# Optimization experiments

Measured on AMD Instinct MI355X. Metric: run time of the kernel, lower is better.

The kernel has to match this reference:

```python
import jax, jax.numpy as jnp
import numpy as np

B, S, ENC, HID = 2, 2048, 2048, 2048
HQ, HKV, D = 8, 4, 256
SOFTCAP = 50.0
SCALING = float(256) ** -0.5  # query_pre_attn_scalar ** -0.5
EPS = 1e-6
NEG = -1e9  # finite stand-in for -inf in additive masks


def _rms_norm(x, w, eps=EPS):
    # GemmaRMSNorm: fp32 compute, scale by (1 + weight)
    xf = x.astype(jnp.float32)
    n = xf * jax.lax.rsqrt(jnp.mean(xf * xf, axis=-1, keepdims=True) + eps)
    return (n * (1.0 + w.astype(jnp.float32))).astype(x.dtype)


def _rotate_half(x):
    x1, x2 = jnp.split(x, 2, axis=-1)
    return jnp.concatenate([-x2, x1], axis=-1)


def _apply_rope(q, k, cos, sin):
    # q,k: [B, H, S, D]; cos,sin: [1, S, D] -> unsqueeze head dim
    c, s = cos[:, None, :, :], sin[:, None, :, :]
    return q * c + _rotate_half(q) * s, k * c + _rotate_half(k) * s


def setup_inputs() -> dict:
    key = jax.random.key(0)
    ks = jax.random.split(key, 8)
    hidden_states = jax.random.normal(ks[0], (B, S, HID), jnp.float32)
    encoder_hidden_states = jax.random.normal(ks[1], (B, ENC, HID), jnp.float32)
    # RoPE tables (base 10000)
    pos = jnp.arange(S, dtype=jnp.float32)
    inv_freq = 1.0 / (10000.0 ** (jnp.arange(0, D, 2, dtype=jnp.float32) / D))
    freqs = pos[:, None] * inv_freq[None, :]                 # [S, D/2]
    emb = jnp.concatenate([freqs, freqs], axis=-1)           # [S, D]
    cos = jnp.cos(emb)[None]                                 # [1, S, D]
    sin = jnp.sin(emb)[None]
    # merged additive mask: causal over self part, fully visible cross part
    causal = jnp.where(jnp.arange(S)[:, None] >= jnp.arange(S)[None, :], 0.0, NEG)
    mask = jnp.concatenate([causal, jnp.zeros((S, ENC), jnp.float32)], axis=-1)
    merged_attention_mask = mask[None, None].astype(jnp.float32)  # [1,1,S,S+ENC]
    w = 0.02
    Wq = jax.random.normal(ks[2], (HQ * D, HID), jnp.float32) * w
    Wk = jax.random.normal(ks[3], (HKV * D, HID), jnp.float32) * w
    Wv = jax.random.normal(ks[4], (HKV * D, HID), jnp.float32) * w
    Wo = jax.random.normal(ks[5], (HID, HQ * D), jnp.float32) * w
    q_norm_w = jnp.zeros((D,), jnp.float32)
    k_norm_w = jnp.zeros((D,), jnp.float32)
    return dict(hidden_states=hidden_states, encoder_hidden_states=encoder_hidden_states,
                cos=cos, sin=sin, merged_attention_mask=merged_attention_mask,
                Wq=Wq, Wk=Wk, Wv=Wv, Wo=Wo, q_norm_w=q_norm_w, k_norm_w=k_norm_w)


def reference(hidden_states, encoder_hidden_states, cos, sin, merged_attention_mask,
              Wq, Wk, Wv, Wo, q_norm_w, k_norm_w):
    b, s, _ = hidden_states.shape
    enc = encoder_hidden_states.shape[1]
    n_rep = HQ // HKV
    # projections
    q = hidden_states @ Wq.T                                 # [B,S,HQ*D]
    k_self = hidden_states @ Wk.T
    v_self = hidden_states @ Wv.T
    k_cross = encoder_hidden_states @ Wk.T
    v_cross = encoder_hidden_states @ Wv.T
    q = q.reshape(b, s, HQ, D).transpose(0, 2, 1, 3)         # [B,HQ,S,D]
    k_self = k_self.reshape(b, s, HKV, D).transpose(0, 2, 1, 3)
    v_self = v_self.reshape(b, s, HKV, D).transpose(0, 2, 1, 3)
    k_cross = k_cross.reshape(b, enc, HKV, D).transpose(0, 2, 1, 3)
    v_cross = v_cross.reshape(b, enc, HKV, D).transpose(0, 2, 1, 3)
    # QK RMSNorm + RoPE (RoPE only on self q/k)
    q = _rms_norm(q, q_norm_w)
    k_self = _rms_norm(k_self, k_norm_w)
    k_cross = _rms_norm(k_cross, k_norm_w)
    q, k_self = _apply_rope(q, k_self, cos, sin)
    # merged KV + GQA repeat
    k = jnp.concatenate([k_self, k_cross], axis=2)           # [B,HKV,S+ENC,D]
    v = jnp.concatenate([v_self, v_cross], axis=2)
    k = jnp.repeat(k, n_rep, axis=1)                         # [B,HQ,S+ENC,D]
    v = jnp.repeat(v, n_rep, axis=1)
    # eager softcapped attention
    scores = jnp.einsum('bhqd,bhkd->bhqk', q, k) * SCALING
    scores = SOFTCAP * jnp.tanh(scores / SOFTCAP)
    scores = scores + merged_attention_mask
    probs = jax.nn.softmax(scores, axis=-1)
    attn = jnp.einsum('bhqk,bhkd->bhqd', probs, v)           # [B,HQ,S,D]
    attn = attn.transpose(0, 2, 1, 3).reshape(b, s, HQ * D)
    return attn @ Wo.T
```

## Files before the change

kernel.cpp:

```cpp
#include <hip/hip_runtime.h>
#include <cstdint>

typedef __attribute__((ext_vector_type(8))) short bf16x8;
typedef __attribute__((ext_vector_type(4))) float f32x4;

#define B_ 2
#define S_ 2048
#define ENC_ 2048
#define HID_ 2048
#define HQ_ 8
#define HKV_ 4
#define D_ 256
#define L_ 4096

__device__ __forceinline__ short f2bf(float f) {
  uint32_t u = __builtin_bit_cast(uint32_t, f);
  u = (u + 0x7fffu + ((u >> 16) & 1u)) >> 16;
  return (short)u;
}
__device__ __forceinline__ float bf2f(short s) {
  uint32_t u = ((uint32_t)(uint16_t)s) << 16;
  return __builtin_bit_cast(float, u);
}

__device__ __forceinline__ void llds16(const void* g, void* s) {
  __builtin_amdgcn_global_load_lds(
      (const __attribute__((address_space(1))) void*)(__builtin_bit_cast(uintptr_t, g)),
      (__attribute__((address_space(3))) void*)(uint32_t)(__builtin_bit_cast(uintptr_t, s)),
      16, 0, 0);
}

__global__ __launch_bounds__(256) void cvt_f32_bf16(const float* __restrict__ in,
                                                    short* __restrict__ out, int n) {
  int i = (blockIdx.x * 256 + threadIdx.x) * 4;
  if (i >= n) return;
  float4 v = *(const float4*)(in + i);
  short4 r;
  r.x = f2bf(v.x); r.y = f2bf(v.y); r.z = f2bf(v.z); r.w = f2bf(v.w);
  *(short4*)(out + i) = r;
}

template <int BF16OUT>
__global__ __launch_bounds__(256, 2)
void gemm_bt(const short* __restrict__ A, const short* __restrict__ Bw,
             void* __restrict__ Cout, int M, int N, int K) {
  __shared__ __align__(16) short As[128 * 32];
  __shared__ __align__(16) short Bs[128 * 32];
  const int t = threadIdx.x;
  const int w = t >> 6;
  const int l = t & 63;
  const int lr = l & 15;
  const int lq = l >> 4;
  const int bm = blockIdx.y * 128;
  const int bn = blockIdx.x * 128;
  const int wm = (w & 1) * 64;
  const int wn = (w >> 1) * 64;

  f32x4 acc[4][4];
#pragma unroll
  for (int i = 0; i < 4; i++)
#pragma unroll
    for (int j = 0; j < 4; j++) acc[i][j] = f32x4{0.f, 0.f, 0.f, 0.f};

  const int srow = 32 * w + (l >> 2);
  const int scol = (l & 3) * 8;
  const short* gA = A + (size_t)(bm + srow) * K + scol;
  const short* gB = Bw + (size_t)(bn + srow) * K + scol;
  short* sA = &As[srow * 32 + scol];
  short* sB = &Bs[srow * 32 + scol];

  for (int k0 = 0; k0 < K; k0 += 32) {
    llds16(gA + k0, sA);
    llds16(gA + k0 + (size_t)16 * K, sA + 16 * 32);
    llds16(gB + k0, sB);
    llds16(gB + k0 + (size_t)16 * K, sB + 16 * 32);
    __syncthreads();
    bf16x8 af[4], bfr[4];
#pragma unroll
    for (int mi = 0; mi < 4; mi++)
      af[mi] = *(const bf16x8*)&As[(wm + 16 * mi + lr) * 32 + lq * 8];
#pragma unroll
    for (int ni = 0; ni < 4; ni++)
      bfr[ni] = *(const bf16x8*)&Bs[(wn + 16 * ni + lr) * 32 + lq * 8];
    __syncthreads();
#pragma unroll
    for (int mi = 0; mi < 4; mi++)
#pragma unroll
      for (int ni = 0; ni < 4; ni++)
        acc[mi][ni] =
            __builtin_amdgcn_mfma_f32_16x16x32_bf16(af[mi], bfr[ni], acc[mi][ni], 0, 0, 0);
  }

#pragma unroll
  for (int mi = 0; mi < 4; mi++)
#pragma unroll
    for (int ni = 0; ni < 4; ni++)
#pragma unroll
      for (int r = 0; r < 4; r++) {
        int row = bm + wm + 16 * mi + lq * 4 + r;
        int col = bn + wn + 16 * ni + lr;
        float v = acc[mi][ni][r];
        if (BF16OUT)
          ((short*)Cout)[(size_t)row * N + col] = f2bf(v);
        else
          ((float*)Cout)[(size_t)row * N + col] = v;
      }
}

__global__ __launch_bounds__(256)
void norm_rope(const short* __restrict__ src, int src_ld, int col0, int H,
               short* __restrict__ dst, int dstL, int pos_off, int do_rope, int kswz,
               const float* __restrict__ wn, const float* __restrict__ cosp,
               const float* __restrict__ sinp) {
  __shared__ float sh[256];
  __shared__ float red[4];
  int bid = blockIdx.x;
  int s = bid & (S_ - 1);
  int h = (bid >> 11) % H;
  int b = (bid >> 11) / H;
  int d = threadIdx.x;
  int w = d >> 6, l = d & 63;
  float x = bf2f(src[(size_t)(b * S_ + s) * src_ld + col0 + h * D_ + d]);
  float ss = x * x;
#pragma unroll
  for (int off = 32; off; off >>= 1) ss += __shfl_xor(ss, off, 64);
  if (l == 0) red[w] = ss;
  __syncthreads();
  float tot = red[0] + red[1] + red[2] + red[3];
  float y = x * rsqrtf(tot * (1.0f / D_) + 1e-6f) * (1.0f + wn[d]);
  float outv = y;
  if (do_rope) {
    sh[d] = y;
    __syncthreads();
    float c = cosp[s * D_ + d];
    float sn = sinp[s * D_ + d];
    outv = (d < 128) ? (y * c - sh[d + 128] * sn) : (y * c + sh[d - 128] * sn);
  }
  int dd = d;
  if (kswz) dd = (((d >> 3) ^ (s & 7)) << 3) | (d & 7);
  dst[((size_t)(b * H + h) * dstL + pos_off + s) * D_ + dd] = f2bf(outv);
}

__global__ __launch_bounds__(256)
void v_transpose(const short* __restrict__ qkv_self, const short* __restrict__ kv_cross,
                 short* __restrict__ Vt) {
  __shared__ __align__(16) short tile[64][72];
  int bid = blockIdx.x;
  int dt = bid & 3;
  int lt = (bid >> 2) & 63;
  int h = (bid >> 8) & 3;
  int b = bid >> 10;
  int t = threadIdx.x;
  int rl = t >> 2;
  int cc = (t & 3) * 16;
  int l = lt * 64 + rl;
  const short* src;
  if (lt < 32)
    src = qkv_self + (size_t)(b * S_ + l) * 4096 + 3072 + h * D_ + dt * 64 + cc;
  else
    src = kv_cross + (size_t)(b * ENC_ + (l - S_)) * 2048 + 1024 + h * D_ + dt * 64 + cc;
  *(bf16x8*)&tile[rl][cc] = *(const bf16x8*)src;
  *(bf16x8*)&tile[rl][cc + 8] = *(const bf16x8*)(src + 8);
  __syncthreads();
  int dl = t >> 2;
  int lc = (t & 3) * 16;
  bf16x8 v0, v1;
#pragma unroll
  for (int j = 0; j < 8; j++) {
    v0[j] = tile[lc + j][dl];
    v1[j] = tile[lc + 8 + j][dl];
  }
  int d = dt * 64 + dl;
  int e = dl & 7;
  int c0 = 2 * (t & 3);
  short* rowp = Vt + ((size_t)(b * HKV_ + h) * D_ + d) * (size_t)L_ + lt * 64;
  *(bf16x8*)(rowp + ((c0 ^ e) * 8)) = v0;
  *(bf16x8*)(rowp + (((c0 + 1) ^ e) * 8)) = v1;
}

__global__ __launch_bounds__(256)
void flash_attn(const short* __restrict__ Q, const short* __restrict__ K,
                const short* __restrict__ Vt, short* __restrict__ part0,
                short* __restrict__ part1, float* __restrict__ lsum) {
  __shared__ __align__(16) short Ks[64 * 256];
  __shared__ __align__(16) short Vs[256 * 64];
  __shared__ __align__(16) short Ps[4][16 * 72];
  int t = threadIdx.x, w = t >> 6, l = t & 63;
  int lr = l & 15, lq = l >> 4, x7 = lr & 7;
  int bid = blockIdx.x;
  int pair = bid >> 5;
  int p = (bid >> 4) & 1;
  int bh = bid & 15;
  int b = bh >> 3, h = bh & 7, hk = h >> 1;
  short* op = p ? part1 : part0;

  const short* Kbase = K + (size_t)(b * HKV_ + hk) * L_ * D_;
  const short* Vbase = Vt + (size_t)(b * HKV_ + hk) * (size_t)D_ * L_;

  int gi = p;
  const int lenA = pair + 33;

  for (int phase = 0; phase < 2; ++phase) {
    int qt = phase ? (31 - pair) : pair;
    int q0 = qt * 64;
    int nself = qt + 1;
    int base = phase ? lenA : 0;
    int lim = base + nself + 32;
    int qglob = q0 + 16 * w + lr;

    bf16x8 qf[8];
    {
      const short* qb = Q + ((size_t)(b * HQ_ + h) * S_ + qglob) * D_ + lq * 8;
#pragma unroll
      for (int kf = 0; kf < 8; kf++) qf[kf] = *(const bf16x8*)(qb + kf * 32);
    }
    f32x4 o[16];
#pragma unroll
    for (int i = 0; i < 16; i++) o[i] = f32x4{0.f, 0.f, 0.f, 0.f};
    float lacc = 0.f;

    for (; gi < lim; gi += 2) {
      int local = gi - base;
      int j = (local < nself) ? local : (local - nself + 32);
      int k0 = j * 64;
      bool diag = (j == qt);

      {
        const short* kg = Kbase + (size_t)(k0 + 16 * w) * 256 + l * 8;
        short* ks = &Ks[16 * w * 256];
#pragma unroll
        for (int i = 0; i < 8; i++) llds16(kg + i * 512, ks + i * 512);
        const short* vg = Vbase + (size_t)(64 * w + (l >> 3)) * L_ + k0 + (l & 7) * 8;
        short* vs = &Vs[64 * w * 64];
#pragma unroll
        for (int i = 0; i < 8; i++) llds16(vg + (size_t)(8 * i) * L_, vs + i * 512);
      }
      __syncthreads();

      f32x4 sc[4];
#pragma unroll
      for (int nt = 0; nt < 4; nt++) sc[nt] = f32x4{0.f, 0.f, 0.f, 0.f};
#pragma unroll
      for (int kf = 0; kf < 8; kf++) {
#pragma unroll
        for (int nt = 0; nt < 4; nt++) {
          bf16x8 a = *(const bf16x8*)&Ks[(nt * 16 + lr) * 256 + (((4 * kf + lq) ^ x7) * 8)];
          sc[nt] = __builtin_amdgcn_mfma_f32_16x16x32_bf16(a, qf[kf], sc[nt], 0, 0, 0);
        }
      }

#pragma unroll
      for (int nt = 0; nt < 4; nt++) {
        float pe[4];
#pragma unroll
        for (int r = 0; r < 4; r++) {
          float s = sc[nt][r];
          float u = s * (1.0f / 800.0f);
          float t2 = u * u;
          float poly = 1.0f + t2 * (-0.33333334f + t2 * (0.13333334f + t2 * (-0.05396825f)));
          float cap = s * 0.0625f * poly;
          float pv = __expf(cap);
          if (diag && (k0 + nt * 16 + 4 * lq + r > qglob)) pv = 0.f;
          pe[r] = pv;
          lacc += pv;
        }
        uint32_t lo = (uint32_t)(uint16_t)f2bf(pe[0]) | ((uint32_t)(uint16_t)f2bf(pe[1]) << 16);
        uint32_t hi = (uint32_t)(uint16_t)f2bf(pe[2]) | ((uint32_t)(uint16_t)f2bf(pe[3]) << 16);
        *(uint2*)&Ps[w][lr * 72 + nt * 16 + lq * 4] = uint2{lo, hi};
      }

#pragma unroll
      for (int kf2 = 0; kf2 < 2; kf2++) {
        bf16x8 pb = *(const bf16x8*)&Ps[w][lr * 72 + kf2 * 32 + lq * 8];
#pragma unroll
        for (int dt = 0; dt < 16; dt++) {
          bf16x8 va = *(const bf16x8*)&Vs[(dt * 16 + lr) * 64 + (((4 * kf2 + lq) ^ x7) * 8)];
          o[dt] = __builtin_amdgcn_mfma_f32_16x16x32_bf16(va, pb, o[dt], 0, 0, 0);
        }
      }
      __syncthreads();
    }

    size_t orow = ((size_t)b * S_ + qglob) * (HQ_ * D_) + h * D_;
#pragma unroll
    for (int dt = 0; dt < 16; dt++) {
      short4 st;
      st.x = f2bf(o[dt][0]);
      st.y = f2bf(o[dt][1]);
      st.z = f2bf(o[dt][2]);
      st.w = f2bf(o[dt][3]);
      *(short4*)(op + orow + dt * 16 + 4 * lq) = st;
    }
    float lrow = lacc;
    lrow += __shfl_xor(lrow, 16, 64);
    lrow += __shfl_xor(lrow, 32, 64);
    if (lq == 0)
      lsum[(((size_t)p * B_ + b) * HQ_ + h) * S_ + qglob] = lrow;
  }
}

__global__ __launch_bounds__(256)
void combine2(const short* __restrict__ p0, const short* __restrict__ p1,
              const float* __restrict__ lsum, short* __restrict__ out) {
  int tid = blockIdx.x * 256 + threadIdx.x;
  int flat = tid * 4;
  int h = (flat >> 8) & 7;
  int s = (flat >> 11) & 2047;
  int b = flat >> 22;
  size_t sbase = ((size_t)b * HQ_ + h) * S_ + s;
  const size_t SP = (size_t)B_ * HQ_ * S_;
  float inv = 1.0f / (lsum[sbase] + lsum[SP + sbase]);
  short4 a = *(const short4*)(p0 + (size_t)flat);
  short4 c = *(const short4*)(p1 + (size_t)flat);
  short4 r;
  r.x = f2bf((bf2f(a.x) + bf2f(c.x)) * inv);
  r.y = f2bf((bf2f(a.y) + bf2f(c.y)) * inv);
  r.z = f2bf((bf2f(a.z) + bf2f(c.z)) * inv);
  r.w = f2bf((bf2f(a.w) + bf2f(c.w)) * inv);
  *(short4*)(out + flat) = r;
}

extern "C" void kernel_launch(void* const* d_in, const int* in_sizes, int n_in, void* d_out,
                              int out_size, void* d_ws, size_t ws_size, hipStream_t stream) {
  (void)in_sizes; (void)n_in; (void)out_size; (void)ws_size;
  const float* hidden = (const float*)d_in[0];
  const float* encoder = (const float*)d_in[1];
  const float* cosp = (const float*)d_in[2];
  const float* sinp = (const float*)d_in[3];
  const float* Wq = (const float*)d_in[5];
  const float* Wk = (const float*)d_in[6];
  const float* Wv = (const float*)d_in[7];
  const float* Wo = (const float*)d_in[8];
  const float* qnw = (const float*)d_in[9];
  const float* knw = (const float*)d_in[10];

  short* ws = (short*)d_ws;
  short* hs_bf = ws;
  short* enc_bf = ws + 8388608;
  short* wqkv_bf = ws + 16777216;
  short* wo_bf = ws + 25165824;
  short* qkv_self = ws + 29360128;
  short* kv_cross = ws + 46137344;
  short* Kb = ws + 54525952;
  short* Vtb = ws + 62914560;
  short* attn_b = hs_bf;
  short* Qb = enc_bf;
  short* part0 = qkv_self;
  short* part1 = qkv_self + 8388608;
  float* lsum = (float*)d_out;

  cvt_f32_bf16<<<8192, 256, 0, stream>>>(hidden, hs_bf, 8388608);
  cvt_f32_bf16<<<8192, 256, 0, stream>>>(encoder, enc_bf, 8388608);
  cvt_f32_bf16<<<4096, 256, 0, stream>>>(Wq, wqkv_bf, 4194304);
  cvt_f32_bf16<<<2048, 256, 0, stream>>>(Wk, wqkv_bf + 4194304, 2097152);
  cvt_f32_bf16<<<2048, 256, 0, stream>>>(Wv, wqkv_bf + 6291456, 2097152);
  cvt_f32_bf16<<<4096, 256, 0, stream>>>(Wo, wo_bf, 4194304);

  gemm_bt<1><<<dim3(32, 32), 256, 0, stream>>>(hs_bf, wqkv_bf, qkv_self, 4096, 4096, 2048);
  gemm_bt<1><<<dim3(16, 32), 256, 0, stream>>>(enc_bf, wqkv_bf + (size_t)2048 * 2048, kv_cross,
                                               4096, 2048, 2048);

  norm_rope<<<32768, 256, 0, stream>>>(qkv_self, 4096, 0, 8, Qb, 2048, 0, 1, 0, qnw, cosp, sinp);
  norm_rope<<<16384, 256, 0, stream>>>(qkv_self, 4096, 2048, 4, Kb, 4096, 0, 1, 1, knw, cosp, sinp);
  norm_rope<<<16384, 256, 0, stream>>>(kv_cross, 2048, 0, 4, Kb, 4096, 2048, 0, 1, knw, cosp, sinp);

  v_transpose<<<2048, 256, 0, stream>>>(qkv_self, kv_cross, Vtb);

  flash_attn<<<512, 256, 0, stream>>>(Qb, Kb, Vtb, part0, part1, lsum);
  combine2<<<8192, 256, 0, stream>>>(part0, part1, lsum, attn_b);

  gemm_bt<0><<<dim3(16, 32), 256, 0, stream>>>(attn_b, wo_bf, d_out, 4096, 2048, 2048);
}
```

Before: 593.3 us.

## Process both query tiles per K/V load in flash attention; vectorize norm_rope

The flash attention kernel now holds both paired query tiles (A and B) in registers at once. Each loaded K/V block is used for both tiles instead of being streamed twice in two phases, which roughly halves K/V global loads and LDS staging. The P buffer is enlarged to two XOR-swizzled tiles, and launch bounds request 2 blocks per CU. The doubled accumulator and Q fragment registers risk spills or lower occupancy. Separately, norm_rope now handles one row per wavefront with 4 elements per lane, using shuffles instead of LDS and barriers.

```diff
diff --git a/kernel.cpp b/kernel.cpp
--- a/kernel.cpp
+++ b/kernel.cpp
@@ -112,33 +112,42 @@
                short* __restrict__ dst, int dstL, int pos_off, int do_rope, int kswz,
                const float* __restrict__ wn, const float* __restrict__ cosp,
                const float* __restrict__ sinp) {
-  __shared__ float sh[256];
-  __shared__ float red[4];
-  int bid = blockIdx.x;
-  int s = bid & (S_ - 1);
-  int h = (bid >> 11) % H;
-  int b = (bid >> 11) / H;
-  int d = threadIdx.x;
-  int w = d >> 6, l = d & 63;
-  float x = bf2f(src[(size_t)(b * S_ + s) * src_ld + col0 + h * D_ + d]);
-  float ss = x * x;
+  int t = threadIdx.x, w = t >> 6, l = t & 63;
+  int r = blockIdx.x * 4 + w;
+  int s = r & (S_ - 1);
+  int h = (r >> 11) % H;
+  int b = (r >> 11) / H;
+  int d0 = 4 * l;
+  short4 xi = *(const short4*)(src + (size_t)(b * S_ + s) * src_ld + col0 + h * D_ + d0);
+  float x[4] = {bf2f(xi.x), bf2f(xi.y), bf2f(xi.z), bf2f(xi.w)};
+  float ss = x[0] * x[0] + x[1] * x[1] + x[2] * x[2] + x[3] * x[3];
 #pragma unroll
   for (int off = 32; off; off >>= 1) ss += __shfl_xor(ss, off, 64);
-  if (l == 0) red[w] = ss;
-  __syncthreads();
-  float tot = red[0] + red[1] + red[2] + red[3];
-  float y = x * rsqrtf(tot * (1.0f / D_) + 1e-6f) * (1.0f + wn[d]);
-  float outv = y;
+  float rs = rsqrtf(ss * (1.0f / D_) + 1e-6f);
+  float4 wv = *(const float4*)(wn + d0);
+  float y[4];
+  y[0] = x[0] * rs * (1.0f + wv.x);
+  y[1] = x[1] * rs * (1.0f + wv.y);
+  y[2] = x[2] * rs * (1.0f + wv.z);
+  y[3] = x[3] * rs * (1.0f + wv.w);
+  float o[4] = {y[0], y[1], y[2], y[3]};
   if (do_rope) {
-    sh[d] = y;
-    __syncthreads();
-    float c = cosp[s * D_ + d];
-    float sn = sinp[s * D_ + d];
-    outv = (d < 128) ? (y * c - sh[d + 128] * sn) : (y * c + sh[d - 128] * sn);
-  }
-  int dd = d;
-  if (kswz) dd = (((d >> 3) ^ (s & 7)) << 3) | (d & 7);
-  dst[((size_t)(b * H + h) * dstL + pos_off + s) * D_ + dd] = f2bf(outv);
+    float4 c = *(const float4*)(cosp + s * D_ + d0);
+    float4 sn = *(const float4*)(sinp + s * D_ + d0);
+    float pr[4];
+#pragma unroll
+    for (int i = 0; i < 4; i++) pr[i] = __shfl_xor(y[i], 32, 64);
+    float sgn = (l < 32) ? -1.f : 1.f;
+    o[0] = y[0] * c.x + sgn * pr[0] * sn.x;
+    o[1] = y[1] * c.y + sgn * pr[1] * sn.y;
+    o[2] = y[2] * c.z + sgn * pr[2] * sn.z;
+    o[3] = y[3] * c.w + sgn * pr[3] * sn.w;
+  }
+  short4 st;
+  st.x = f2bf(o[0]); st.y = f2bf(o[1]); st.z = f2bf(o[2]); st.w = f2bf(o[3]);
+  int dd = d0;
+  if (kswz) dd = ((((l >> 1) ^ (s & 7)) * 8) | ((l & 1) * 4));
+  *(short4*)(dst + ((size_t)(b * H + h) * dstL + pos_off + s) * D_ + dd) = st;
 }
 
 __global__ __launch_bounds__(256)
@@ -178,13 +187,13 @@
   *(bf16x8*)(rowp + (((c0 + 1) ^ e) * 8)) = v1;
 }
 
-__global__ __launch_bounds__(256)
+__global__ __launch_bounds__(256, 2)
 void flash_attn(const short* __restrict__ Q, const short* __restrict__ K,
                 const short* __restrict__ Vt, short* __restrict__ part0,
                 short* __restrict__ part1, float* __restrict__ lsum) {
   __shared__ __align__(16) short Ks[64 * 256];
   __shared__ __align__(16) short Vs[256 * 64];
-  __shared__ __align__(16) short Ps[4][16 * 72];
+  __shared__ __align__(16) short Ps[4][2][1024];
   int t = threadIdx.x, w = t >> 6, l = t & 63;
   int lr = l & 15, lq = l >> 4, x7 = lr & 7;
   int bid = blockIdx.x;
@@ -197,58 +206,81 @@
   const short* Kbase = K + (size_t)(b * HKV_ + hk) * L_ * D_;
   const short* Vbase = Vt + (size_t)(b * HKV_ + hk) * (size_t)D_ * L_;
 
-  int gi = p;
-  const int lenA = pair + 33;
-
-  for (int phase = 0; phase < 2; ++phase) {
-    int qt = phase ? (31 - pair) : pair;
-    int q0 = qt * 64;
-    int nself = qt + 1;
-    int base = phase ? lenA : 0;
-    int lim = base + nself + 32;
-    int qglob = q0 + 16 * w + lr;
-
-    bf16x8 qf[8];
+  const int qtA = pair, qtB = 31 - pair;
+  const int qglobA = qtA * 64 + 16 * w + lr;
+  const int qglobB = qtB * 64 + 16 * w + lr;
+
+  bf16x8 qfA[8], qfB[8];
+  {
+    const short* qa = Q + ((size_t)(b * HQ_ + h) * S_ + qglobA) * D_ + lq * 8;
+    const short* qb = Q + ((size_t)(b * HQ_ + h) * S_ + qglobB) * D_ + lq * 8;
+#pragma unroll
+    for (int kf = 0; kf < 8; kf++) {
+      qfA[kf] = *(const bf16x8*)(qa + kf * 32);
+      qfB[kf] = *(const bf16x8*)(qb + kf * 32);
+    }
+  }
+  f32x4 oA[16], oB[16];
+#pragma unroll
+  for (int i = 0; i < 16; i++) {
+    oA[i] = f32x4{0.f, 0.f, 0.f, 0.f};
+    oB[i] = f32x4{0.f, 0.f, 0.f, 0.f};
+  }
+  float laccA = 0.f, laccB = 0.f;
+  short* psw = &Ps[w][0][0];
+
+  const int nselfB = qtB + 1;
+  const int lenB = nselfB + 32;
+  for (int local = p; local < lenB; local += 2) {
+    int j = (local < nselfB) ? local : (local - nselfB + 32);
+    int k0 = j * 64;
+    bool Aact = (j <= qtA) || (j >= 32);
+    bool diagA = (j == qtA), diagB = (j == qtB);
+
     {
-      const short* qb = Q + ((size_t)(b * HQ_ + h) * S_ + qglob) * D_ + lq * 8;
-#pragma unroll
-      for (int kf = 0; kf < 8; kf++) qf[kf] = *(const bf16x8*)(qb + kf * 32);
-    }
-    f32x4 o[16];
-#pragma unroll
-    for (int i = 0; i < 16; i++) o[i] = f32x4{0.f, 0.f, 0.f, 0.f};
-    float lacc = 0.f;
-
-    for (; gi < lim; gi += 2) {
-      int local = gi - base;
-      int j = (local < nself) ? local : (local - nself + 32);
-      int k0 = j * 64;
-      bool diag = (j == qt);
-
-      {
-        const short* kg = Kbase + (size_t)(k0 + 16 * w) * 256 + l * 8;
-        short* ks = &Ks[16 * w * 256];
-#pragma unroll
-        for (int i = 0; i < 8; i++) llds16(kg + i * 512, ks + i * 512);
-        const short* vg = Vbase + (size_t)(64 * w + (l >> 3)) * L_ + k0 + (l & 7) * 8;
-        short* vs = &Vs[64 * w * 64];
-#pragma unroll
-        for (int i = 0; i < 8; i++) llds16(vg + (size_t)(8 * i) * L_, vs + i * 512);
-      }
-      __syncthreads();
-
-      f32x4 sc[4];
-#pragma unroll
-      for (int nt = 0; nt < 4; nt++) sc[nt] = f32x4{0.f, 0.f, 0.f, 0.f};
-#pragma unroll
-      for (int kf = 0; kf < 8; kf++) {
+      const short* kg = Kbase + (size_t)(k0 + 16 * w) * 256 + l * 8;
+      short* ks = &Ks[16 * w * 256];
+#pragma unroll
+      for (int i = 0; i < 8; i++) llds16(kg + i * 512, ks + i * 512);
+      const short* vg = Vbase + (size_t)(64 * w + (l >> 3)) * L_ + k0 + (l & 7) * 8;
+      short* vs = &Vs[64 * w * 64];
+#pragma unroll
+      for (int i = 0; i < 8; i++) llds16(vg + (size_t)(8 * i) * L_, vs + i * 512);
+    }
+    __syncthreads();
+
+    f32x4 scA[4], scB[4];
+#pragma unroll
+    for (int nt = 0; nt < 4; nt++) {
+      scA[nt] = f32x4{0.f, 0.f, 0.f, 0.f};
+      scB[nt] = f32x4{0.f, 0.f, 0.f, 0.f};
+    }
+    if (Aact) {
+#pragma unroll
+      for (int kf = 0; kf < 8; kf++)
 #pragma unroll
         for (int nt = 0; nt < 4; nt++) {
           bf16x8 a = *(const bf16x8*)&Ks[(nt * 16 + lr) * 256 + (((4 * kf + lq) ^ x7) * 8)];
-          sc[nt] = __builtin_amdgcn_mfma_f32_16x16x32_bf16(a, qf[kf], sc[nt], 0, 0, 0);
+          scA[nt] = __builtin_amdgcn_mfma_f32_16x16x32_bf16(a, qfA[kf], scA[nt], 0, 0, 0);
+          scB[nt] = __builtin_amdgcn_mfma_f32_16x16x32_bf16(a, qfB[kf], scB[nt], 0, 0, 0);
         }
-      }
-
+    } else {
+#pragma unroll
+      for (int kf = 0; kf < 8; kf++)
+#pragma unroll
+        for (int nt = 0; nt < 4; nt++) {
+          bf16x8 a = *(const bf16x8*)&Ks[(nt * 16 + lr) * 256 + (((4 * kf + lq) ^ x7) * 8)];
+          scB[nt] = __builtin_amdgcn_mfma_f32_16x16x32_bf16(a, qfB[kf], scB[nt], 0, 0, 0);
+        }
+    }
+
+#pragma unroll
+    for (int tile = 0; tile < 2; tile++) {
+      if (tile == 0 && !Aact) continue;
+      bool dg = tile ? diagB : diagA;
+      int qg = tile ? qglobB : qglobA;
+      f32x4* sc = tile ? scB : scA;
+      float la = 0.f;
 #pragma unroll
       for (int nt = 0; nt < 4; nt++) {
         float pe[4];
@@ -260,28 +292,52 @@
           float poly = 1.0f + t2 * (-0.33333334f + t2 * (0.13333334f + t2 * (-0.05396825f)));
           float cap = s * 0.0625f * poly;
           float pv = __expf(cap);
-          if (diag && (k0 + nt * 16 + 4 * lq + r > qglob)) pv = 0.f;
+          if (dg && (k0 + nt * 16 + 4 * lq + r > qg)) pv = 0.f;
           pe[r] = pv;
-          lacc += pv;
+          la += pv;
         }
         uint32_t lo = (uint32_t)(uint16_t)f2bf(pe[0]) | ((uint32_t)(uint16_t)f2bf(pe[1]) << 16);
         uint32_t hi = (uint32_t)(uint16_t)f2bf(pe[2]) | ((uint32_t)(uint16_t)f2bf(pe[3]) << 16);
-        *(uint2*)&Ps[w][lr * 72 + nt * 16 + lq * 4] = uint2{lo, hi};
+        int off = lr * 64 + (((nt * 2 + (lq >> 1)) ^ x7) * 8) + (lq & 1) * 4;
+        *(uint2*)&psw[tile * 1024 + off] = uint2{lo, hi};
       }
-
+      if (tile) laccB += la; else laccA += la;
+    }
+
+    if (Aact) {
 #pragma unroll
       for (int kf2 = 0; kf2 < 2; kf2++) {
-        bf16x8 pb = *(const bf16x8*)&Ps[w][lr * 72 + kf2 * 32 + lq * 8];
+        int poff = lr * 64 + (((kf2 * 4 + lq) ^ x7) * 8);
+        bf16x8 pA = *(const bf16x8*)&psw[poff];
+        bf16x8 pB = *(const bf16x8*)&psw[1024 + poff];
 #pragma unroll
         for (int dt = 0; dt < 16; dt++) {
           bf16x8 va = *(const bf16x8*)&Vs[(dt * 16 + lr) * 64 + (((4 * kf2 + lq) ^ x7) * 8)];
-          o[dt] = __builtin_amdgcn_mfma_f32_16x16x32_bf16(va, pb, o[dt], 0, 0, 0);
+          oA[dt] = __builtin_amdgcn_mfma_f32_16x16x32_bf16(va, pA, oA[dt], 0, 0, 0);
+          oB[dt] = __builtin_amdgcn_mfma_f32_16x16x32_bf16(va, pB, oB[dt], 0, 0, 0);
         }
       }
-      __syncthreads();
-    }
-
-    size_t orow = ((size_t)b * S_ + qglob) * (HQ_ * D_) + h * D_;
+    } else {
+#pragma unroll
+      for (int kf2 = 0; kf2 < 2; kf2++) {
+        int poff = lr * 64 + (((kf2 * 4 + lq) ^ x7) * 8);
+        bf16x8 pB = *(const bf16x8*)&psw[1024 + poff];
+#pragma unroll
+        for (int dt = 0; dt < 16; dt++) {
+          bf16x8 va = *(const bf16x8*)&Vs[(dt * 16 + lr) * 64 + (((4 * kf2 + lq) ^ x7) * 8)];
+          oB[dt] = __builtin_amdgcn_mfma_f32_16x16x32_bf16(va, pB, oB[dt], 0, 0, 0);
+        }
+      }
+    }
+    __syncthreads();
+  }
+
+#pragma unroll
+  for (int tile = 0; tile < 2; tile++) {
+    int qg = tile ? qglobB : qglobA;
+    f32x4* o = tile ? oB : oA;
+    float la = tile ? laccB : laccA;
+    size_t orow = ((size_t)b * S_ + qg) * (HQ_ * D_) + h * D_;
 #pragma unroll
     for (int dt = 0; dt < 16; dt++) {
       short4 st;
@@ -291,11 +347,11 @@
       st.w = f2bf(o[dt][3]);
       *(short4*)(op + orow + dt * 16 + 4 * lq) = st;
     }
-    float lrow = lacc;
+    float lrow = la;
     lrow += __shfl_xor(lrow, 16, 64);
     lrow += __shfl_xor(lrow, 32, 64);
     if (lq == 0)
-      lsum[(((size_t)p * B_ + b) * HQ_ + h) * S_ + qglob] = lrow;
+      lsum[(((size_t)p * B_ + b) * HQ_ + h) * S_ + qg] = lrow;
   }
 }
 
@@ -360,9 +416,9 @@
   gemm_bt<1><<<dim3(16, 32), 256, 0, stream>>>(enc_bf, wqkv_bf + (size_t)2048 * 2048, kv_cross,
                                                4096, 2048, 2048);
 
-  norm_rope<<<32768, 256, 0, stream>>>(qkv_self, 4096, 0, 8, Qb, 2048, 0, 1, 0, qnw, cosp, sinp);
-  norm_rope<<<16384, 256, 0, stream>>>(qkv_self, 4096, 2048, 4, Kb, 4096, 0, 1, 1, knw, cosp, sinp);
-  norm_rope<<<16384, 256, 0, stream>>>(kv_cross, 2048, 0, 4, Kb, 4096, 2048, 0, 1, knw, cosp, sinp);
+  norm_rope<<<8192, 256, 0, stream>>>(qkv_self, 4096, 0, 8, Qb, 2048, 0, 1, 0, qnw, cosp, sinp);
+  norm_rope<<<4096, 256, 0, stream>>>(qkv_self, 4096, 2048, 4, Kb, 4096, 0, 1, 1, knw, cosp, sinp);
+  norm_rope<<<4096, 256, 0, stream>>>(kv_cross, 2048, 0, 4, Kb, 4096, 2048, 0, 1, knw, cosp, sinp);
 
   v_transpose<<<2048, 256, 0, stream>>>(qkv_self, kv_cross, Vtb);
 
```

Result: slower. 677.8 us (+14.2%).
